# Kernel optimization log

Hardware: AMD Instinct MI355X
Metric: run time of the kernel (lower is better)

The kernel has to match this reference:

```python
import jax, jax.numpy as jnp
import numpy as np

N_EMBD = 1024
N_HEAD = 16
HEAD_SIZE = N_EMBD // N_HEAD
EPS = 1e-5


def _layernorm(x, g, b):
    m = x.mean(-1, keepdims=True)
    v = x.var(-1, keepdims=True)
    return (x - m) / jnp.sqrt(v + EPS) * g + b


def _mha(q_in, kv_in, wq, wk, wv, pw, pb, causal):
    # q_in: [B,T,C], kv_in: [B,S,C]; per-head Linear projections fused into one matmul.
    B, T, C = q_in.shape
    S = kv_in.shape[1]
    H, hd = N_HEAD, HEAD_SIZE
    q = (q_in @ wq).reshape(B, T, H, hd)
    k = (kv_in @ wk).reshape(B, S, H, hd)
    v = (kv_in @ wv).reshape(B, S, H, hd)
    scale = 1.0 / np.sqrt(hd).astype(np.float32)
    wei = jnp.einsum('bthd,bshd->bhts', q, k) * scale  # [B,H,T,S]
    if causal:
        mask = jnp.tril(jnp.ones((T, S), dtype=bool))
        wei = jnp.where(mask, wei, -jnp.inf)
    attn = jax.nn.softmax(wei, axis=-1)
    out = jnp.einsum('bhts,bshd->bthd', attn, v).reshape(B, T, C)
    return out @ pw + pb


def setup_inputs() -> dict:
    key = jax.random.key(0)
    ks = jax.random.split(key, 20)
    C = N_EMBD
    B, T, S = 8, 1024, 1024
    s = 0.02
    inp = {
        'x': jax.random.normal(ks[0], (B, T, C), jnp.float32),
        'encoder_output': jax.random.normal(ks[1], (B, S, C), jnp.float32),
        # self-attention (per-head q/k/v Linears concatenated head-major -> [C, C])
        'sa_wq': jax.random.normal(ks[2], (C, C), jnp.float32) * s,
        'sa_wk': jax.random.normal(ks[3], (C, C), jnp.float32) * s,
        'sa_wv': jax.random.normal(ks[4], (C, C), jnp.float32) * s,
        'sa_pw': jax.random.normal(ks[5], (C, C), jnp.float32) * s,
        'sa_pb': jnp.zeros((C,), jnp.float32),
        # cross-attention
        'ca_wq': jax.random.normal(ks[6], (C, C), jnp.float32) * s,
        'ca_wk': jax.random.normal(ks[7], (C, C), jnp.float32) * s,
        'ca_wv': jax.random.normal(ks[8], (C, C), jnp.float32) * s,
        'ca_pw': jax.random.normal(ks[9], (C, C), jnp.float32) * s,
        'ca_pb': jnp.zeros((C,), jnp.float32),
        # feed-forward
        'ff_w1': jax.random.normal(ks[10], (C, 4 * C), jnp.float32) * s,
        'ff_b1': jnp.zeros((4 * C,), jnp.float32),
        'ff_w2': jax.random.normal(ks[11], (4 * C, C), jnp.float32) * s,
        'ff_b2': jnp.zeros((C,), jnp.float32),
        # layernorms
        'ln1_g': jnp.ones((C,), jnp.float32), 'ln1_b': jnp.zeros((C,), jnp.float32),
        'ln2_g': jnp.ones((C,), jnp.float32), 'ln2_b': jnp.zeros((C,), jnp.float32),
        'ln3_g': jnp.ones((C,), jnp.float32), 'ln3_b': jnp.zeros((C,), jnp.float32),
    }
    return inp


def reference(x, encoder_output, sa_wq, sa_wk, sa_wv, sa_pw, sa_pb,
              ca_wq, ca_wk, ca_wv, ca_pw, ca_pb,
              ff_w1, ff_b1, ff_w2, ff_b2,
              ln1_g, ln1_b, ln2_g, ln2_b, ln3_g, ln3_b):
    # self-attn: q from ln1(x), but k/v from raw residual x (memory=x in source)
    x = x + _mha(_layernorm(x, ln1_g, ln1_b), x, sa_wq, sa_wk, sa_wv, sa_pw, sa_pb, causal=True)
    # cross-attn: q from ln2(x), k/v from encoder_output, no mask
    x = x + _mha(_layernorm(x, ln2_g, ln2_b), encoder_output, ca_wq, ca_wk, ca_wv, ca_pw, ca_pb, causal=False)
    # feed-forward: Linear -> ReLU -> Linear
    h = _layernorm(x, ln3_g, ln3_b)
    x = x + (jax.nn.relu(h @ ff_w1 + ff_b1) @ ff_w2 + ff_b2)
    return x
```

## Files before the change

### kernel.cpp

```cpp
#include <hip/hip_runtime.h>
#include <stdint.h>
#include <stddef.h>

typedef __bf16 bf16_t;
typedef __bf16 bf16x4 __attribute__((ext_vector_type(4)));
typedef __bf16 bf16x8 __attribute__((ext_vector_type(8)));
typedef float f32x4 __attribute__((ext_vector_type(4)));

#define DEV static __device__ __forceinline__

static constexpr int kB = 8, kT = 1024, kC = 1024, kM = 8192, kH = 16, kHD = 64, kFF = 4096;

DEV f32x4 mfma16(bf16x8 a, bf16x8 b, f32x4 c) {
  return __builtin_amdgcn_mfma_f32_16x16x32_bf16(a, b, c, 0, 0, 0);
}

DEV float ex2(float x) {
  float r;
  asm("v_exp_f32 %0, %1" : "=v"(r) : "v"(x));
  return r;
}

DEV void gload_lds16(const void* g, void* l) {
  __builtin_amdgcn_global_load_lds(
      reinterpret_cast<const __attribute__((address_space(1))) void*>(
          reinterpret_cast<uintptr_t>(g)),
      reinterpret_cast<__attribute__((address_space(3))) void*>(
          static_cast<uint32_t>(reinterpret_cast<uintptr_t>(l))),
      16, 0, 0);
}

__global__ void k_cast_bf16(const float* __restrict__ in, bf16_t* __restrict__ out, int n4) {
  int i = blockIdx.x * blockDim.x + threadIdx.x;
  if (i >= n4) return;
  float4 v = reinterpret_cast<const float4*>(in)[i];
  bf16x4 o;
  o[0] = (bf16_t)v.x; o[1] = (bf16_t)v.y; o[2] = (bf16_t)v.z; o[3] = (bf16_t)v.w;
  reinterpret_cast<bf16x4*>(out)[i] = o;
}

struct Trans8Args { const float* src[8]; bf16_t* dst[8]; };
__global__ void k_transpose_cast8(Trans8Args a) {
  __shared__ float tile[32][33];
  const float* __restrict__ in = a.src[blockIdx.z];
  bf16_t* __restrict__ out = a.dst[blockIdx.z];
  int c0 = blockIdx.x * 32, r0 = blockIdx.y * 32;
  int tx = threadIdx.x, ty = threadIdx.y;
#pragma unroll
  for (int i = 0; i < 4; ++i)
    tile[ty + 8 * i][tx] = in[(size_t)(r0 + ty + 8 * i) * kC + c0 + tx];
  __syncthreads();
#pragma unroll
  for (int i = 0; i < 4; ++i)
    out[(size_t)(c0 + ty + 8 * i) * kC + r0 + tx] = (bf16_t)tile[tx][ty + 8 * i];
}

__global__ void k_transpose_cast(const float* __restrict__ in, bf16_t* __restrict__ out,
                                 int R, int C) {
  __shared__ float tile[32][33];
  int c0 = blockIdx.x * 32, r0 = blockIdx.y * 32;
  int tx = threadIdx.x, ty = threadIdx.y;
#pragma unroll
  for (int i = 0; i < 4; ++i)
    tile[ty + 8 * i][tx] = in[(size_t)(r0 + ty + 8 * i) * C + c0 + tx];
  __syncthreads();
#pragma unroll
  for (int i = 0; i < 4; ++i)
    out[(size_t)(c0 + ty + 8 * i) * R + r0 + tx] = (bf16_t)tile[tx][ty + 8 * i];
}

template <bool CASTX>
__global__ __launch_bounds__(256) void k_ln(const float* __restrict__ in,
                                            const float* __restrict__ g,
                                            const float* __restrict__ b,
                                            bf16_t* __restrict__ out,
                                            bf16_t* __restrict__ rawout) {
  int row = blockIdx.x, t = threadIdx.x;
  const float4 v = reinterpret_cast<const float4*>(in + (size_t)row * kC)[t];
  if constexpr (CASTX) {
    bf16x4 c;
    c[0] = (bf16_t)v.x; c[1] = (bf16_t)v.y; c[2] = (bf16_t)v.z; c[3] = (bf16_t)v.w;
    reinterpret_cast<bf16x4*>(rawout + (size_t)row * kC)[t] = c;
  }
  float s = v.x + v.y + v.z + v.w;
  float ss = v.x * v.x + v.y * v.y + v.z * v.z + v.w * v.w;
#pragma unroll
  for (int off = 1; off < 64; off <<= 1) {
    s += __shfl_xor(s, off, 64);
    ss += __shfl_xor(ss, off, 64);
  }
  __shared__ float rs[4], rss[4];
  int w = t >> 6;
  if ((t & 63) == 0) { rs[w] = s; rss[w] = ss; }
  __syncthreads();
  s = rs[0] + rs[1] + rs[2] + rs[3];
  ss = rss[0] + rss[1] + rss[2] + rss[3];
  float mean = s * (1.f / kC);
  float var = ss * (1.f / kC) - mean * mean;
  float rstd = rsqrtf(var + 1e-5f);
  float4 gv = reinterpret_cast<const float4*>(g)[t];
  float4 bv = reinterpret_cast<const float4*>(b)[t];
  bf16x4 o;
  o[0] = (bf16_t)((v.x - mean) * rstd * gv.x + bv.x);
  o[1] = (bf16_t)((v.y - mean) * rstd * gv.y + bv.y);
  o[2] = (bf16_t)((v.z - mean) * rstd * gv.z + bv.z);
  o[3] = (bf16_t)((v.w - mean) * rstd * gv.w + bv.w);
  reinterpret_cast<bf16x4*>(out + (size_t)row * kC)[t] = o;
}

template <int EPI>
__global__ __launch_bounds__(512, 2) void k_gemm2(
    const bf16_t* __restrict__ A, const bf16_t* __restrict__ Bt,
    const float* __restrict__ bias, const float* __restrict__ res,
    float* __restrict__ outf, bf16_t* __restrict__ outb, bf16_t* __restrict__ outb2,
    int M, int N, int K) {
  extern __shared__ bf16_t smem[];
  bf16_t* As = smem;
  bf16_t* Bs = smem + 3 * 8192;
  const int t = threadIdx.x;
  const int w = t >> 6, lane = t & 63;
  const int l15 = lane & 15, l4 = lane >> 4;
  const int wr = w >> 2, wc = w & 3;
  const int bm0 = blockIdx.y * 128, bn0 = blockIdx.x * 256;

  f32x4 acc[4][4] = {};

  const int srow = w * 8 + (lane >> 3);
  const int scol = ((lane & 7) ^ (lane >> 3)) * 8;
  const bf16_t* aSrc0 = A + (size_t)(bm0 + srow) * K + scol;
  const bf16_t* bSrc0 = Bt + (size_t)(bn0 + srow) * K + scol;
  const size_t r64 = (size_t)64 * K;

  const int arow = wr * 64 + l15;
  const int brow = wc * 64 + l15;
  const int cbx = (l15 & 7) * 16;
  const int cbe0 = ((l4 * 16) ^ cbx) >> 1;
  const int cbe1 = ((64 | (l4 * 16)) ^ cbx) >> 1;

  const int nkt = K >> 6;

  auto stage = [&](int tt, int bi) {
    const size_t ko = (size_t)tt * 64;
    bf16_t* da = As + bi * 8192;
    bf16_t* db = Bs + bi * 16384;
    gload_lds16(aSrc0 + ko,            da + w * 512);
    gload_lds16(aSrc0 + ko + r64,      da + 4096 + w * 512);
    gload_lds16(bSrc0 + ko,            db + w * 512);
    gload_lds16(bSrc0 + ko + r64,      db + 4096 + w * 512);
    gload_lds16(bSrc0 + ko + 2 * r64,  db + 8192 + w * 512);
    gload_lds16(bSrc0 + ko + 3 * r64,  db + 12288 + w * 512);
  };

  stage(0, 0);
  stage(1, 1);
  asm volatile("s_waitcnt vmcnt(6)" ::: "memory");
  __builtin_amdgcn_s_barrier();

  int bi = 0, bs = 2;
  for (int tt = 0; tt < nkt; ++tt) {
    if (tt + 2 < nkt) stage(tt + 2, bs);
    const bf16_t* bA = As + bi * 8192;
    const bf16_t* bB = Bs + bi * 16384;
    bf16x8 af[4], bfr[4];
#pragma unroll
    for (int m = 0; m < 4; ++m)
      af[m] = *reinterpret_cast<const bf16x8*>(&bA[(arow + m * 16) * 64 + cbe0]);
#pragma unroll
    for (int n = 0; n < 4; ++n)
      bfr[n] = *reinterpret_cast<const bf16x8*>(&bB[(brow + n * 16) * 64 + cbe0]);
    __builtin_amdgcn_s_setprio(1);
#pragma unroll
    for (int m = 0; m < 4; ++m)
#pragma unroll
      for (int n = 0; n < 4; ++n) acc[m][n] = mfma16(af[m], bfr[n], acc[m][n]);
    __builtin_amdgcn_s_setprio(0);
#pragma unroll
    for (int m = 0; m < 4; ++m)
      af[m] = *reinterpret_cast<const bf16x8*>(&bA[(arow + m * 16) * 64 + cbe1]);
#pragma unroll
    for (int n = 0; n < 4; ++n)
      bfr[n] = *reinterpret_cast<const bf16x8*>(&bB[(brow + n * 16) * 64 + cbe1]);
    __builtin_amdgcn_s_setprio(1);
#pragma unroll
    for (int m = 0; m < 4; ++m)
#pragma unroll
      for (int n = 0; n < 4; ++n) acc[m][n] = mfma16(af[m], bfr[n], acc[m][n]);
    __builtin_amdgcn_s_setprio(0);
    if (tt + 1 < nkt) {
      if (tt + 2 < nkt) asm volatile("s_waitcnt vmcnt(6)" ::: "memory");
      else              asm volatile("s_waitcnt vmcnt(0)" ::: "memory");
      __builtin_amdgcn_s_barrier();
    }
    bi = (bi == 2) ? 0 : bi + 1;
    bs = (bs == 2) ? 0 : bs + 1;
  }

  const int gm = bm0 + wr * 64 + l4 * 4;
  const int gn = bn0 + wc * 64 + l15;
  if constexpr (EPI == 0) {
#pragma unroll
    for (int m = 0; m < 4; ++m)
#pragma unroll
      for (int n = 0; n < 4; ++n)
#pragma unroll
        for (int r = 0; r < 4; ++r)
          outb[(size_t)(gm + m * 16 + r) * N + (gn + n * 16)] = (bf16_t)acc[m][n][r];
  } else if constexpr (EPI == 1) {
#pragma unroll
    for (int m = 0; m < 4; ++m)
#pragma unroll
      for (int n = 0; n < 4; ++n) {
        const int col = gn + n * 16;
        const float bv = bias[col];
#pragma unroll
        for (int r = 0; r < 4; ++r) {
          const size_t idx = (size_t)(gm + m * 16 + r) * N + col;
          outf[idx] = acc[m][n][r] + bv + res[idx];
        }
      }
  } else if constexpr (EPI == 2) {
#pragma unroll
    for (int m = 0; m < 4; ++m)
#pragma unroll
      for (int n = 0; n < 4; ++n) {
        const int col = gn + n * 16;
        const float bv = bias[col];
#pragma unroll
        for (int r = 0; r < 4; ++r) {
          float v = acc[m][n][r] + bv;
          v = fmaxf(v, 0.f);
          outb[(size_t)(gm + m * 16 + r) * N + col] = (bf16_t)v;
        }
      }
  } else if constexpr (EPI == 3) {
#pragma unroll
    for (int m = 0; m < 4; ++m)
#pragma unroll
      for (int n = 0; n < 4; ++n) {
        bf16x4 ov;
#pragma unroll
        for (int r = 0; r < 4; ++r) ov[r] = (bf16_t)acc[m][n][r];
        *reinterpret_cast<bf16x4*>(&outb[(size_t)(gn + n * 16) * M + gm + m * 16]) = ov;
      }
  } else {
    const int half = N >> 1;
    if (bn0 < half) {
#pragma unroll
      for (int m = 0; m < 4; ++m)
#pragma unroll
        for (int n = 0; n < 4; ++n)
#pragma unroll
          for (int r = 0; r < 4; ++r)
            outb[(size_t)(gm + m * 16 + r) * half + (gn + n * 16)] = (bf16_t)acc[m][n][r];
    } else {
#pragma unroll
      for (int m = 0; m < 4; ++m)
#pragma unroll
        for (int n = 0; n < 4; ++n) {
          bf16x4 ov;
#pragma unroll
          for (int r = 0; r < 4; ++r) ov[r] = (bf16_t)acc[m][n][r];
          *reinterpret_cast<bf16x4*>(
              &outb2[(size_t)(gn + n * 16 - half) * M + gm + m * 16]) = ov;
        }
    }
  }
}

template <bool CAUSAL>
__global__ __launch_bounds__(256) void k_attn(const bf16_t* __restrict__ Q,
                                              const bf16_t* __restrict__ Kb,
                                              const bf16_t* __restrict__ Vt,
                                              bf16_t* __restrict__ O) {
  __shared__ bf16_t Ks[2][4096];
  __shared__ bf16_t Vs[2][4096];
  __shared__ bf16_t P[4][32][72];
  const int b = blockIdx.x, h = blockIdx.y;
  const int w = threadIdx.x >> 6, lane = threadIdx.x & 63;
  const int l15 = lane & 15, l4 = lane >> 4;
  const int qblk = CAUSAL ? (kT / 128 - 1 - blockIdx.z) : blockIdx.z;
  const int qr0 = qblk * 128 + w * 32;

  bf16x8 qf[2][2];
#pragma unroll
  for (int a = 0; a < 2; ++a) {
    const bf16_t* qp = Q + (size_t)(b * kT + qr0 + a * 16 + l15) * kC + h * kHD + l4 * 8;
    qf[a][0] = *reinterpret_cast<const bf16x8*>(qp);
    qf[a][1] = *reinterpret_cast<const bf16x8*>(qp + 32);
#pragma unroll
    for (int j = 0; j < 8; ++j) {
      qf[a][0][j] = (bf16_t)((float)qf[a][0][j] * 0.1803368801111204f);
      qf[a][1][j] = (bf16_t)((float)qf[a][1][j] * 0.1803368801111204f);
    }
  }
  bf16x8 ones;
#pragma unroll
  for (int j = 0; j < 8; ++j) ones[j] = (bf16_t)1.0f;

  f32x4 po[2][4] = {};
  f32x4 po_s[2] = {};
  float mrun[2];
  mrun[0] = mrun[1] = -3.0e38f;

  const int nkt = CAUSAL ? 2 * qblk + 2 : (kT / 64);
  const int klim = CAUSAL ? ((qr0 + 31) >> 6) : (1 << 30);

  const int lr = lane >> 3;
  const int cswz = ((lane & 7) ^ lr) * 8;
  const bf16_t* kSrc0 = Kb + (size_t)(b * kT + 2 * w * 8 + lr) * kC + h * kHD + cswz;
  const bf16_t* kSrc1 = Kb + (size_t)(b * kT + (2 * w + 1) * 8 + lr) * kC + h * kHD + cswz;
  const bf16_t* vSrc0 = Vt + (size_t)(h * kHD + 2 * w * 8 + lr) * (kB * kT) + b * kT + cswz;
  const bf16_t* vSrc1 = Vt + (size_t)(h * kHD + (2 * w + 1) * 8 + lr) * (kB * kT) + b * kT + cswz;

  auto stage = [&](int kt, int buf) {
    const size_t kk = (size_t)kt * 64 * kC;
    const size_t vv = (size_t)kt * 64;
    gload_lds16(kSrc0 + kk, &Ks[buf][(2 * w) * 512]);
    gload_lds16(kSrc1 + kk, &Ks[buf][(2 * w + 1) * 512]);
    gload_lds16(vSrc0 + vv, &Vs[buf][(2 * w) * 512]);
    gload_lds16(vSrc1 + vv, &Vs[buf][(2 * w + 1) * 512]);
  };

  const int cbx = (l15 & 7) * 16;
  const int rb0 = ((l4 * 16) ^ cbx) >> 1;
  const int rb1 = ((64 | (l4 * 16)) ^ cbx) >> 1;

  stage(0, 0);
  asm volatile("s_waitcnt vmcnt(0)" ::: "memory");
  __builtin_amdgcn_s_barrier();

  int buf = 0;
  for (int kt = 0; kt < nkt; ++kt) {
    if (kt + 1 < nkt) stage(kt + 1, buf ^ 1);
    if (kt <= klim) {
      bf16x8 kf[4][2];
#pragma unroll
      for (int sub = 0; sub < 4; ++sub) {
        kf[sub][0] = *reinterpret_cast<const bf16x8*>(&Ks[buf][(sub * 16 + l15) * 64 + rb0]);
        kf[sub][1] = *reinterpret_cast<const bf16x8*>(&Ks[buf][(sub * 16 + l15) * 64 + rb1]);
      }
      bf16x8 vf[2][4];
#pragma unroll
      for (int n = 0; n < 4; ++n) {
        vf[0][n] = *reinterpret_cast<const bf16x8*>(&Vs[buf][(n * 16 + l15) * 64 + rb0]);
        vf[1][n] = *reinterpret_cast<const bf16x8*>(&Vs[buf][(n * 16 + l15) * 64 + rb1]);
      }

      f32x4 s[2][4] = {};
      __builtin_amdgcn_s_setprio(1);
#pragma unroll
      for (int a = 0; a < 2; ++a)
#pragma unroll
        for (int sub = 0; sub < 4; ++sub) {
          s[a][sub] = mfma16(kf[sub][0], qf[a][0], s[a][sub]);
          s[a][sub] = mfma16(kf[sub][1], qf[a][1], s[a][sub]);
        }
      __builtin_amdgcn_s_setprio(0);
      if (CAUSAL && kt == klim) {
#pragma unroll
        for (int a = 0; a < 2; ++a) {
          const int qrow = qr0 + a * 16 + l15;
#pragma unroll
          for (int sub = 0; sub < 4; ++sub)
#pragma unroll
            for (int r = 0; r < 4; ++r) {
              const int key = kt * 64 + sub * 16 + l4 * 4 + r;
              if (key > qrow) s[a][sub][r] = -3.0e38f;
            }
        }
      }
#pragma unroll
      for (int a = 0; a < 2; ++a) {
        float t0 = fmaxf(fmaxf(s[a][0][0], s[a][0][1]), fmaxf(s[a][0][2], s[a][0][3]));
        float t1 = fmaxf(fmaxf(s[a][1][0], s[a][1][1]), fmaxf(s[a][1][2], s[a][1][3]));
        float t2 = fmaxf(fmaxf(s[a][2][0], s[a][2][1]), fmaxf(s[a][2][2], s[a][2][3]));
        float t3 = fmaxf(fmaxf(s[a][3][0], s[a][3][1]), fmaxf(s[a][3][2], s[a][3][3]));
        float v = fmaxf(fmaxf(t0, t1), fmaxf(t2, t3));
        v = fmaxf(v, __shfl_xor(v, 16, 64));
        v = fmaxf(v, __shfl_xor(v, 32, 64));
        if (!__all(v <= mrun[a] + 8.f)) {
          const float mnew = fmaxf(mrun[a], v);
          const float corr = ex2(mrun[a] - mnew);
          mrun[a] = mnew;
#pragma unroll
          for (int n = 0; n < 4; ++n)
#pragma unroll
            for (int r = 0; r < 4; ++r) po[a][n][r] *= corr;
#pragma unroll
          for (int r = 0; r < 4; ++r) po_s[a][r] *= corr;
        }
#pragma unroll
        for (int sub = 0; sub < 4; ++sub) {
          bf16x4 pk;
#pragma unroll
          for (int r = 0; r < 4; ++r) pk[r] = (bf16_t)ex2(s[a][sub][r] - mrun[a]);
          *reinterpret_cast<bf16x4*>(&P[w][a * 16 + l15][sub * 16 + l4 * 4]) = pk;
        }
      }
#pragma unroll
      for (int a = 0; a < 2; ++a)
#pragma unroll
        for (int kk = 0; kk < 2; ++kk) {
          const bf16x8 pf =
              *reinterpret_cast<const bf16x8*>(&P[w][a * 16 + l15][kk * 32 + l4 * 8]);
          __builtin_amdgcn_s_setprio(1);
#pragma unroll
          for (int n = 0; n < 4; ++n) po[a][n] = mfma16(vf[kk][n], pf, po[a][n]);
          po_s[a] = mfma16(ones, pf, po_s[a]);
          __builtin_amdgcn_s_setprio(0);
        }
    }
    asm volatile("s_waitcnt vmcnt(0)" ::: "memory");
    __builtin_amdgcn_s_barrier();
    buf ^= 1;
  }

#pragma unroll
  for (int a = 0; a < 2; ++a) {
    const float inv = 1.f / po_s[a][0];
#pragma unroll
    for (int n = 0; n < 4; ++n) {
      bf16x4 ov;
#pragma unroll
      for (int r = 0; r < 4; ++r) ov[r] = (bf16_t)(po[a][n][r] * inv);
      *reinterpret_cast<bf16x4*>(
          O + (size_t)(b * kT + qr0 + a * 16 + l15) * kC + h * kHD + n * 16 + l4 * 4) = ov;
    }
  }
}

extern "C" void kernel_launch(void* const* d_in, const int* in_sizes, int n_in,
                              void* d_out, int out_size, void* d_ws, size_t ws_size,
                              hipStream_t stream) {
  const float* x      = (const float*)d_in[0];
  const float* enc    = (const float*)d_in[1];
  const float* sa_wq  = (const float*)d_in[2];
  const float* sa_wk  = (const float*)d_in[3];
  const float* sa_wv  = (const float*)d_in[4];
  const float* sa_pw  = (const float*)d_in[5];
  const float* sa_pb  = (const float*)d_in[6];
  const float* ca_wq  = (const float*)d_in[7];
  const float* ca_wk  = (const float*)d_in[8];
  const float* ca_wv  = (const float*)d_in[9];
  const float* ca_pw  = (const float*)d_in[10];
  const float* ca_pb  = (const float*)d_in[11];
  const float* ff_w1  = (const float*)d_in[12];
  const float* ff_b1  = (const float*)d_in[13];
  const float* ff_w2  = (const float*)d_in[14];
  const float* ff_b2  = (const float*)d_in[15];
  const float* ln1_g  = (const float*)d_in[16];
  const float* ln1_b  = (const float*)d_in[17];
  const float* ln2_g  = (const float*)d_in[18];
  const float* ln2_b  = (const float*)d_in[19];
  const float* ln3_g  = (const float*)d_in[20];
  const float* ln3_b  = (const float*)d_in[21];

  const size_t ACT_BF = (size_t)kM * kC * 2;
  const size_t ACT_F  = (size_t)kM * kC * 4;
  const size_t W_BF   = (size_t)kC * kC * 2;
  const size_t FF_BF  = (size_t)kC * kFF * 2;
  const size_t H_BF   = (size_t)kM * kFF * 2;

  char* ws = (char*)d_ws;
  size_t off = 0;
  auto alloc = [&](size_t bytes) {
    char* p = ws + off;
    off += (bytes + 255) & ~(size_t)255;
    return p;
  };
  bf16_t* xbf   = (bf16_t*)alloc(ACT_BF);
  bf16_t* encbf = (bf16_t*)alloc(ACT_BF);
  bf16_t* lnbuf = (bf16_t*)alloc(ACT_BF);
  bf16_t* wsaq  = (bf16_t*)alloc(W_BF);
  bf16_t* wkvsa = (bf16_t*)alloc(2 * W_BF);
  bf16_t* wsap  = (bf16_t*)alloc(W_BF);
  bf16_t* wcaq  = (bf16_t*)alloc(W_BF);
  bf16_t* wkvca = (bf16_t*)alloc(2 * W_BF);
  bf16_t* wcap  = (bf16_t*)alloc(W_BF);
  bf16_t* wff1t = (bf16_t*)alloc(FF_BF);
  bf16_t* wff2t = (bf16_t*)alloc(FF_BF);
  float*  rbuf  = (float*)alloc(ACT_F);
  char*   scr   = alloc(5 * ACT_BF > H_BF ? 5 * ACT_BF : H_BF);
  bf16_t* qbf   = (bf16_t*)scr;
  bf16_t* kbf   = (bf16_t*)(scr + ACT_BF);
  bf16_t* vtbf  = (bf16_t*)(scr + 3 * ACT_BF);
  bf16_t* aobf  = (bf16_t*)(scr + 4 * ACT_BF);
  bf16_t* hbf   = (bf16_t*)scr;

  const dim3 blk512(512), blk256(256), blkT(32, 8);
  const int n4 = kM * kC / 4;
  const dim3 gGemmC(kC / 256, kM / 128);
  const dim3 gGemmKV(2 * kC / 256, kM / 128);
  const dim3 gGemmF(kFF / 256, kM / 128);
  const dim3 gAttn(kB, kH, kT / 128);
  const uint32_t LDSB = 147456;

  hipFuncSetAttribute((const void*)k_gemm2<0>, hipFuncAttributeMaxDynamicSharedMemorySize, LDSB);
  hipFuncSetAttribute((const void*)k_gemm2<1>, hipFuncAttributeMaxDynamicSharedMemorySize, LDSB);
  hipFuncSetAttribute((const void*)k_gemm2<2>, hipFuncAttributeMaxDynamicSharedMemorySize, LDSB);
  hipFuncSetAttribute((const void*)k_gemm2<4>, hipFuncAttributeMaxDynamicSharedMemorySize, LDSB);

  k_cast_bf16<<<n4 / 256, blk256, 0, stream>>>(enc, encbf, n4);
  Trans8Args ta;
  ta.src[0] = sa_wq; ta.dst[0] = wsaq;
  ta.src[1] = sa_wk; ta.dst[1] = wkvsa;
  ta.src[2] = sa_wv; ta.dst[2] = wkvsa + (size_t)kC * kC;
  ta.src[3] = sa_pw; ta.dst[3] = wsap;
  ta.src[4] = ca_wq; ta.dst[4] = wcaq;
  ta.src[5] = ca_wk; ta.dst[5] = wkvca;
  ta.src[6] = ca_wv; ta.dst[6] = wkvca + (size_t)kC * kC;
  ta.src[7] = ca_pw; ta.dst[7] = wcap;
  k_transpose_cast8<<<dim3(kC / 32, kC / 32, 8), blkT, 0, stream>>>(ta);
  k_transpose_cast<<<dim3(kFF / 32, kC / 32), blkT, 0, stream>>>(ff_w1, wff1t, kC, kFF);
  k_transpose_cast<<<dim3(kC / 32, kFF / 32), blkT, 0, stream>>>(ff_w2, wff2t, kFF, kC);

  k_ln<true><<<kM, blk256, 0, stream>>>(x, ln1_g, ln1_b, lnbuf, xbf);
  k_gemm2<0><<<gGemmC, blk512, LDSB, stream>>>(lnbuf, wsaq, nullptr, nullptr, nullptr, qbf, nullptr, kM, kC, kC);
  k_gemm2<4><<<gGemmKV, blk512, LDSB, stream>>>(xbf, wkvsa, nullptr, nullptr, nullptr, kbf, vtbf, kM, 2 * kC, kC);
  k_attn<true><<<gAttn, blk256, 0, stream>>>(qbf, kbf, vtbf, aobf);
  k_gemm2<1><<<gGemmC, blk512, LDSB, stream>>>(aobf, wsap, sa_pb, x, rbuf, nullptr, nullptr, kM, kC, kC);

  k_ln<false><<<kM, blk256, 0, stream>>>(rbuf, ln2_g, ln2_b, lnbuf, nullptr);
  k_gemm2<0><<<gGemmC, blk512, LDSB, stream>>>(lnbuf, wcaq, nullptr, nullptr, nullptr, qbf, nullptr, kM, kC, kC);
  k_gemm2<4><<<gGemmKV, blk512, LDSB, stream>>>(encbf, wkvca, nullptr, nullptr, nullptr, kbf, vtbf, kM, 2 * kC, kC);
  k_attn<false><<<gAttn, blk256, 0, stream>>>(qbf, kbf, vtbf, aobf);
  k_gemm2<1><<<gGemmC, blk512, LDSB, stream>>>(aobf, wcap, ca_pb, rbuf, rbuf, nullptr, nullptr, kM, kC, kC);

  k_ln<false><<<kM, blk256, 0, stream>>>(rbuf, ln3_g, ln3_b, lnbuf, nullptr);
  k_gemm2<2><<<gGemmF, blk512, LDSB, stream>>>(lnbuf, wff1t, ff_b1, nullptr, nullptr, hbf, nullptr, kM, kFF, kC);
  k_gemm2<1><<<gGemmC, blk512, LDSB, stream>>>(hbf, wff2t, ff_b2, rbuf, (float*)d_out, nullptr, nullptr, kM, kC, kFF);

  (void)in_sizes; (void)n_in; (void)out_size; (void)ws_size;
}
```

Baseline: 515.0 us.

## Add 256x256-tile GEMM kernel with split-half pipelining for KV and FF1 projections

Introduces k_gemm3, a 256x256 output tile GEMM with 8 waves (each computing 128x64) that double-buffers A and B in LDS and stages the next K tile in four quarter loads interleaved with MFMA phases. It replaces the 128-row k_gemm2 for the wide KV projections and the FF1 layer, aiming to raise arithmetic intensity and cut global/LDS traffic per FLOP. The larger accumulator footprint (128 floats per thread) raises register pressure and halves the grid size, which could hurt occupancy or tail balance.

```diff
diff --git a/kernel.cpp b/kernel.cpp
--- a/kernel.cpp
+++ b/kernel.cpp
@@ -255,6 +255,172 @@
     } else {
 #pragma unroll
       for (int m = 0; m < 4; ++m)
+#pragma unroll
+        for (int n = 0; n < 4; ++n) {
+          bf16x4 ov;
+#pragma unroll
+          for (int r = 0; r < 4; ++r) ov[r] = (bf16_t)acc[m][n][r];
+          *reinterpret_cast<bf16x4*>(
+              &outb2[(size_t)(gn + n * 16 - half) * M + gm + m * 16]) = ov;
+        }
+    }
+  }
+}
+
+template <int EPI>
+__global__ __launch_bounds__(512, 2) void k_gemm3(
+    const bf16_t* __restrict__ A, const bf16_t* __restrict__ Bt,
+    const float* __restrict__ bias,
+    bf16_t* __restrict__ outb, bf16_t* __restrict__ outb2,
+    int M, int N, int K) {
+  extern __shared__ bf16_t smem[];
+  bf16_t* As = smem;
+  bf16_t* Bs = smem + 32768;
+  const int t = threadIdx.x;
+  const int w = t >> 6, lane = t & 63;
+  const int l15 = lane & 15, l4 = lane >> 4;
+  const int wr = w >> 2, wc = w & 3;
+  const int bm0 = blockIdx.y * 256, bn0 = blockIdx.x * 256;
+
+  f32x4 acc[8][4] = {};
+
+  const int srow = w * 8 + (lane >> 3);
+  const int scol = ((lane & 7) ^ (lane >> 3)) * 8;
+  const bf16_t* aSrc0 = A + (size_t)(bm0 + srow) * K + scol;
+  const bf16_t* bSrc0 = Bt + (size_t)(bn0 + srow) * K + scol;
+  const size_t r64 = (size_t)64 * K;
+
+  const int arow = wr * 128 + l15;
+  const int brow = wc * 64 + l15;
+  const int cbx = (l15 & 7) * 16;
+  const int cbe0 = ((l4 * 16) ^ cbx) >> 1;
+  const int cbe1 = ((64 | (l4 * 16)) ^ cbx) >> 1;
+
+  const int nkt = K >> 6;
+
+  auto stage_half = [&](int tt, int h, int bi) {
+    const size_t ko = (size_t)tt * 64;
+    if (h < 2) {
+      bf16_t* d = As + bi * 16384 + h * 8192 + w * 512;
+      gload_lds16(aSrc0 + ko + (size_t)(2 * h) * r64,     d);
+      gload_lds16(aSrc0 + ko + (size_t)(2 * h + 1) * r64, d + 4096);
+    } else {
+      const int hh = h - 2;
+      bf16_t* d = Bs + bi * 16384 + hh * 8192 + w * 512;
+      gload_lds16(bSrc0 + ko + (size_t)(2 * hh) * r64,     d);
+      gload_lds16(bSrc0 + ko + (size_t)(2 * hh + 1) * r64, d + 4096);
+    }
+  };
+
+  stage_half(0, 0, 0); stage_half(0, 1, 0); stage_half(0, 2, 0); stage_half(0, 3, 0);
+  if (nkt > 1) {
+    stage_half(1, 0, 1); stage_half(1, 1, 1);
+    asm volatile("s_waitcnt vmcnt(4)" ::: "memory");
+  } else {
+    asm volatile("s_waitcnt vmcnt(0)" ::: "memory");
+  }
+  __builtin_amdgcn_s_barrier();
+
+  for (int tt = 0; tt < nkt; ++tt) {
+    const int bi = tt & 1;
+    const bf16_t* bA = As + bi * 16384;
+    const bf16_t* bB = Bs + bi * 16384;
+    bf16x8 aK0lo[4], aK0hi[4], aK1lo[4], aK1hi[4], bK0[4], bK1[4];
+
+#pragma unroll
+    for (int m = 0; m < 4; ++m)
+      aK0lo[m] = *reinterpret_cast<const bf16x8*>(&bA[(arow + m * 16) * 64 + cbe0]);
+#pragma unroll
+    for (int n = 0; n < 4; ++n)
+      bK0[n] = *reinterpret_cast<const bf16x8*>(&bB[(brow + n * 16) * 64 + cbe0]);
+    if (tt + 1 < nkt) stage_half(tt + 1, 2, bi ^ 1);
+    __builtin_amdgcn_s_barrier();
+    asm volatile("s_waitcnt lgkmcnt(0)" ::: "memory");
+    __builtin_amdgcn_s_setprio(1);
+#pragma unroll
+    for (int m = 0; m < 4; ++m)
+#pragma unroll
+      for (int n = 0; n < 4; ++n) acc[m][n] = mfma16(aK0lo[m], bK0[n], acc[m][n]);
+    __builtin_amdgcn_s_setprio(0);
+    __builtin_amdgcn_s_barrier();
+
+#pragma unroll
+    for (int m = 0; m < 4; ++m)
+      aK0hi[m] = *reinterpret_cast<const bf16x8*>(&bA[(arow + 64 + m * 16) * 64 + cbe0]);
+    if (tt + 1 < nkt) stage_half(tt + 1, 3, bi ^ 1);
+    __builtin_amdgcn_s_barrier();
+    asm volatile("s_waitcnt lgkmcnt(0)" ::: "memory");
+    __builtin_amdgcn_s_setprio(1);
+#pragma unroll
+    for (int m = 0; m < 4; ++m)
+#pragma unroll
+      for (int n = 0; n < 4; ++n) acc[4 + m][n] = mfma16(aK0hi[m], bK0[n], acc[4 + m][n]);
+    __builtin_amdgcn_s_setprio(0);
+    __builtin_amdgcn_s_barrier();
+
+#pragma unroll
+    for (int m = 0; m < 4; ++m)
+      aK1lo[m] = *reinterpret_cast<const bf16x8*>(&bA[(arow + m * 16) * 64 + cbe1]);
+#pragma unroll
+    for (int m = 0; m < 4; ++m)
+      aK1hi[m] = *reinterpret_cast<const bf16x8*>(&bA[(arow + 64 + m * 16) * 64 + cbe1]);
+#pragma unroll
+    for (int n = 0; n < 4; ++n)
+      bK1[n] = *reinterpret_cast<const bf16x8*>(&bB[(brow + n * 16) * 64 + cbe1]);
+    __builtin_amdgcn_s_barrier();
+    asm volatile("s_waitcnt lgkmcnt(0)" ::: "memory");
+    __builtin_amdgcn_s_setprio(1);
+#pragma unroll
+    for (int m = 0; m < 4; ++m)
+#pragma unroll
+      for (int n = 0; n < 4; ++n) acc[m][n] = mfma16(aK1lo[m], bK1[n], acc[m][n]);
+    __builtin_amdgcn_s_setprio(0);
+    __builtin_amdgcn_s_barrier();
+
+    if (tt + 2 < nkt) { stage_half(tt + 2, 0, bi); stage_half(tt + 2, 1, bi); }
+    if (tt + 1 < nkt) {
+      if (tt + 2 < nkt) asm volatile("s_waitcnt vmcnt(4)" ::: "memory");
+      else              asm volatile("s_waitcnt vmcnt(0)" ::: "memory");
+    }
+    __builtin_amdgcn_s_barrier();
+    __builtin_amdgcn_s_setprio(1);
+#pragma unroll
+    for (int m = 0; m < 4; ++m)
+#pragma unroll
+      for (int n = 0; n < 4; ++n) acc[4 + m][n] = mfma16(aK1hi[m], bK1[n], acc[4 + m][n]);
+    __builtin_amdgcn_s_setprio(0);
+    __builtin_amdgcn_s_barrier();
+  }
+
+  const int gm = bm0 + wr * 128 + l4 * 4;
+  const int gn = bn0 + wc * 64 + l15;
+  if constexpr (EPI == 2) {
+#pragma unroll
+    for (int m = 0; m < 8; ++m)
+#pragma unroll
+      for (int n = 0; n < 4; ++n) {
+        const int col = gn + n * 16;
+        const float bv = bias[col];
+#pragma unroll
+        for (int r = 0; r < 4; ++r) {
+          float v = acc[m][n][r] + bv;
+          v = fmaxf(v, 0.f);
+          outb[(size_t)(gm + m * 16 + r) * N + col] = (bf16_t)v;
+        }
+      }
+  } else {
+    const int half = N >> 1;
+    if (bn0 < half) {
+#pragma unroll
+      for (int m = 0; m < 8; ++m)
+#pragma unroll
+        for (int n = 0; n < 4; ++n)
+#pragma unroll
+          for (int r = 0; r < 4; ++r)
+            outb[(size_t)(gm + m * 16 + r) * half + (gn + n * 16)] = (bf16_t)acc[m][n][r];
+    } else {
+#pragma unroll
+      for (int m = 0; m < 8; ++m)
 #pragma unroll
         for (int n = 0; n < 4; ++n) {
           bf16x4 ov;
@@ -490,15 +656,17 @@
   const dim3 blk512(512), blk256(256), blkT(32, 8);
   const int n4 = kM * kC / 4;
   const dim3 gGemmC(kC / 256, kM / 128);
-  const dim3 gGemmKV(2 * kC / 256, kM / 128);
-  const dim3 gGemmF(kFF / 256, kM / 128);
+  const dim3 gGemmF2(kC / 256, kM / 128);
+  const dim3 gKV3(2 * kC / 256, kM / 256);
+  const dim3 gFF13(kFF / 256, kM / 256);
   const dim3 gAttn(kB, kH, kT / 128);
-  const uint32_t LDSB = 147456;
-
-  hipFuncSetAttribute((const void*)k_gemm2<0>, hipFuncAttributeMaxDynamicSharedMemorySize, LDSB);
-  hipFuncSetAttribute((const void*)k_gemm2<1>, hipFuncAttributeMaxDynamicSharedMemorySize, LDSB);
-  hipFuncSetAttribute((const void*)k_gemm2<2>, hipFuncAttributeMaxDynamicSharedMemorySize, LDSB);
-  hipFuncSetAttribute((const void*)k_gemm2<4>, hipFuncAttributeMaxDynamicSharedMemorySize, LDSB);
+  const uint32_t LDSB2 = 147456;
+  const uint32_t LDSB3 = 131072;
+
+  hipFuncSetAttribute((const void*)k_gemm2<0>, hipFuncAttributeMaxDynamicSharedMemorySize, LDSB2);
+  hipFuncSetAttribute((const void*)k_gemm2<1>, hipFuncAttributeMaxDynamicSharedMemorySize, LDSB2);
+  hipFuncSetAttribute((const void*)k_gemm3<2>, hipFuncAttributeMaxDynamicSharedMemorySize, LDSB3);
+  hipFuncSetAttribute((const void*)k_gemm3<4>, hipFuncAttributeMaxDynamicSharedMemorySize, LDSB3);
 
   k_cast_bf16<<<n4 / 256, blk256, 0, stream>>>(enc, encbf, n4);
   Trans8Args ta;
@@ -515,20 +683,20 @@
   k_transpose_cast<<<dim3(kC / 32, kFF / 32), blkT, 0, stream>>>(ff_w2, wff2t, kFF, kC);
 
   k_ln<true><<<kM, blk256, 0, stream>>>(x, ln1_g, ln1_b, lnbuf, xbf);
-  k_gemm2<0><<<gGemmC, blk512, LDSB, stream>>>(lnbuf, wsaq, nullptr, nullptr, nullptr, qbf, nullptr, kM, kC, kC);
-  k_gemm2<4><<<gGemmKV, blk512, LDSB, stream>>>(xbf, wkvsa, nullptr, nullptr, nullptr, kbf, vtbf, kM, 2 * kC, kC);
+  k_gemm2<0><<<gGemmC, blk512, LDSB2, stream>>>(lnbuf, wsaq, nullptr, nullptr, nullptr, qbf, nullptr, kM, kC, kC);
+  k_gemm3<4><<<gKV3, blk512, LDSB3, stream>>>(xbf, wkvsa, nullptr, kbf, vtbf, kM, 2 * kC, kC);
   k_attn<true><<<gAttn, blk256, 0, stream>>>(qbf, kbf, vtbf, aobf);
-  k_gemm2<1><<<gGemmC, blk512, LDSB, stream>>>(aobf, wsap, sa_pb, x, rbuf, nullptr, nullptr, kM, kC, kC);
+  k_gemm2<1><<<gGemmC, blk512, LDSB2, stream>>>(aobf, wsap, sa_pb, x, rbuf, nullptr, nullptr, kM, kC, kC);
 
   k_ln<false><<<kM, blk256, 0, stream>>>(rbuf, ln2_g, ln2_b, lnbuf, nullptr);
-  k_gemm2<0><<<gGemmC, blk512, LDSB, stream>>>(lnbuf, wcaq, nullptr, nullptr, nullptr, qbf, nullptr, kM, kC, kC);
-  k_gemm2<4><<<gGemmKV, blk512, LDSB, stream>>>(encbf, wkvca, nullptr, nullptr, nullptr, kbf, vtbf, kM, 2 * kC, kC);
+  k_gemm2<0><<<gGemmC, blk512, LDSB2, stream>>>(lnbuf, wcaq, nullptr, nullptr, nullptr, qbf, nullptr, kM, kC, kC);
+  k_gemm3<4><<<gKV3, blk512, LDSB3, stream>>>(encbf, wkvca, nullptr, kbf, vtbf, kM, 2 * kC, kC);
   k_attn<false><<<gAttn, blk256, 0, stream>>>(qbf, kbf, vtbf, aobf);
-  k_gemm2<1><<<gGemmC, blk512, LDSB, stream>>>(aobf, wcap, ca_pb, rbuf, rbuf, nullptr, nullptr, kM, kC, kC);
+  k_gemm2<1><<<gGemmC, blk512, LDSB2, stream>>>(aobf, wcap, ca_pb, rbuf, rbuf, nullptr, nullptr, kM, kC, kC);
 
   k_ln<false><<<kM, blk256, 0, stream>>>(rbuf, ln3_g, ln3_b, lnbuf, nullptr);
-  k_gemm2<2><<<gGemmF, blk512, LDSB, stream>>>(lnbuf, wff1t, ff_b1, nullptr, nullptr, hbf, nullptr, kM, kFF, kC);
-  k_gemm2<1><<<gGemmC, blk512, LDSB, stream>>>(hbf, wff2t, ff_b2, rbuf, (float*)d_out, nullptr, nullptr, kM, kC, kFF);
+  k_gemm3<2><<<gFF13, blk512, LDSB3, stream>>>(lnbuf, wff1t, ff_b1, hbf, nullptr, kM, kFF, kC);
+  k_gemm2<1><<<gGemmF2, blk512, LDSB2, stream>>>(hbf, wff2t, ff_b2, rbuf, (float*)d_out, nullptr, nullptr, kM, kC, kFF);
 
   (void)in_sizes; (void)n_in; (void)out_size; (void)ws_size;
 }
```

Result: faster. 504.5 us (-2.1%).

## Shrink GEMM tile to 128x128 with 4 waves and double buffering

Applied to the files above, without the earlier changes.

The GEMM kernel moves from a 128x256 tile with 8 waves and triple-buffered LDS to a 128x128 tile with 4 waves and double buffering. LDS use drops from 147456 to 65536 bytes, so more blocks can be resident per CU and the grid doubles in size. The cost is less operand reuse per loaded byte and a shallower prefetch pipeline that waits with vmcnt(0) every iteration, which may expose global-load latency.

```diff
diff --git a/kernel.cpp b/kernel.cpp
--- a/kernel.cpp
+++ b/kernel.cpp
@@ -109,19 +109,19 @@
 }
 
 template <int EPI>
-__global__ __launch_bounds__(512, 2) void k_gemm2(
+__global__ __launch_bounds__(256, 2) void k_gemm2(
     const bf16_t* __restrict__ A, const bf16_t* __restrict__ Bt,
     const float* __restrict__ bias, const float* __restrict__ res,
     float* __restrict__ outf, bf16_t* __restrict__ outb, bf16_t* __restrict__ outb2,
     int M, int N, int K) {
   extern __shared__ bf16_t smem[];
   bf16_t* As = smem;
-  bf16_t* Bs = smem + 3 * 8192;
+  bf16_t* Bs = smem + 2 * 8192;
   const int t = threadIdx.x;
   const int w = t >> 6, lane = t & 63;
   const int l15 = lane & 15, l4 = lane >> 4;
-  const int wr = w >> 2, wc = w & 3;
-  const int bm0 = blockIdx.y * 128, bn0 = blockIdx.x * 256;
+  const int wr = w >> 1, wc = w & 1;
+  const int bm0 = blockIdx.y * 128, bn0 = blockIdx.x * 128;
 
   f32x4 acc[4][4] = {};
 
@@ -129,7 +129,7 @@
   const int scol = ((lane & 7) ^ (lane >> 3)) * 8;
   const bf16_t* aSrc0 = A + (size_t)(bm0 + srow) * K + scol;
   const bf16_t* bSrc0 = Bt + (size_t)(bn0 + srow) * K + scol;
-  const size_t r64 = (size_t)64 * K;
+  const size_t r32 = (size_t)32 * K;
 
   const int arow = wr * 64 + l15;
   const int brow = wc * 64 + l15;
@@ -141,26 +141,24 @@
 
   auto stage = [&](int tt, int bi) {
     const size_t ko = (size_t)tt * 64;
-    bf16_t* da = As + bi * 8192;
-    bf16_t* db = Bs + bi * 16384;
-    gload_lds16(aSrc0 + ko,            da + w * 512);
-    gload_lds16(aSrc0 + ko + r64,      da + 4096 + w * 512);
-    gload_lds16(bSrc0 + ko,            db + w * 512);
-    gload_lds16(bSrc0 + ko + r64,      db + 4096 + w * 512);
-    gload_lds16(bSrc0 + ko + 2 * r64,  db + 8192 + w * 512);
-    gload_lds16(bSrc0 + ko + 3 * r64,  db + 12288 + w * 512);
+    bf16_t* da = As + bi * 8192 + w * 512;
+    bf16_t* db = Bs + bi * 8192 + w * 512;
+#pragma unroll
+    for (int c = 0; c < 4; ++c) {
+      gload_lds16(aSrc0 + ko + (size_t)c * r32, da + c * 2048);
+      gload_lds16(bSrc0 + ko + (size_t)c * r32, db + c * 2048);
+    }
   };
 
   stage(0, 0);
-  stage(1, 1);
-  asm volatile("s_waitcnt vmcnt(6)" ::: "memory");
+  asm volatile("s_waitcnt vmcnt(0)" ::: "memory");
   __builtin_amdgcn_s_barrier();
 
-  int bi = 0, bs = 2;
+  int bi = 0;
   for (int tt = 0; tt < nkt; ++tt) {
-    if (tt + 2 < nkt) stage(tt + 2, bs);
+    if (tt + 1 < nkt) stage(tt + 1, bi ^ 1);
     const bf16_t* bA = As + bi * 8192;
-    const bf16_t* bB = Bs + bi * 16384;
+    const bf16_t* bB = Bs + bi * 8192;
     bf16x8 af[4], bfr[4];
 #pragma unroll
     for (int m = 0; m < 4; ++m)
@@ -187,12 +185,10 @@
       for (int n = 0; n < 4; ++n) acc[m][n] = mfma16(af[m], bfr[n], acc[m][n]);
     __builtin_amdgcn_s_setprio(0);
     if (tt + 1 < nkt) {
-      if (tt + 2 < nkt) asm volatile("s_waitcnt vmcnt(6)" ::: "memory");
-      else              asm volatile("s_waitcnt vmcnt(0)" ::: "memory");
+      asm volatile("s_waitcnt vmcnt(0)" ::: "memory");
       __builtin_amdgcn_s_barrier();
     }
-    bi = (bi == 2) ? 0 : bi + 1;
-    bs = (bs == 2) ? 0 : bs + 1;
+    bi ^= 1;
   }
 
   const int gm = bm0 + wr * 64 + l4 * 4;
@@ -487,13 +483,13 @@
   bf16_t* aobf  = (bf16_t*)(scr + 4 * ACT_BF);
   bf16_t* hbf   = (bf16_t*)scr;
 
-  const dim3 blk512(512), blk256(256), blkT(32, 8);
+  const dim3 blk256(256), blkT(32, 8);
   const int n4 = kM * kC / 4;
-  const dim3 gGemmC(kC / 256, kM / 128);
-  const dim3 gGemmKV(2 * kC / 256, kM / 128);
-  const dim3 gGemmF(kFF / 256, kM / 128);
+  const dim3 gGemmC(kC / 128, kM / 128);
+  const dim3 gGemmKV(2 * kC / 128, kM / 128);
+  const dim3 gGemmF(kFF / 128, kM / 128);
   const dim3 gAttn(kB, kH, kT / 128);
-  const uint32_t LDSB = 147456;
+  const uint32_t LDSB = 65536;
 
   hipFuncSetAttribute((const void*)k_gemm2<0>, hipFuncAttributeMaxDynamicSharedMemorySize, LDSB);
   hipFuncSetAttribute((const void*)k_gemm2<1>, hipFuncAttributeMaxDynamicSharedMemorySize, LDSB);
@@ -515,20 +511,20 @@
   k_transpose_cast<<<dim3(kC / 32, kFF / 32), blkT, 0, stream>>>(ff_w2, wff2t, kFF, kC);
 
   k_ln<true><<<kM, blk256, 0, stream>>>(x, ln1_g, ln1_b, lnbuf, xbf);
-  k_gemm2<0><<<gGemmC, blk512, LDSB, stream>>>(lnbuf, wsaq, nullptr, nullptr, nullptr, qbf, nullptr, kM, kC, kC);
-  k_gemm2<4><<<gGemmKV, blk512, LDSB, stream>>>(xbf, wkvsa, nullptr, nullptr, nullptr, kbf, vtbf, kM, 2 * kC, kC);
+  k_gemm2<0><<<gGemmC, blk256, LDSB, stream>>>(lnbuf, wsaq, nullptr, nullptr, nullptr, qbf, nullptr, kM, kC, kC);
+  k_gemm2<4><<<gGemmKV, blk256, LDSB, stream>>>(xbf, wkvsa, nullptr, nullptr, nullptr, kbf, vtbf, kM, 2 * kC, kC);
   k_attn<true><<<gAttn, blk256, 0, stream>>>(qbf, kbf, vtbf, aobf);
-  k_gemm2<1><<<gGemmC, blk512, LDSB, stream>>>(aobf, wsap, sa_pb, x, rbuf, nullptr, nullptr, kM, kC, kC);
+  k_gemm2<1><<<gGemmC, blk256, LDSB, stream>>>(aobf, wsap, sa_pb, x, rbuf, nullptr, nullptr, kM, kC, kC);
 
   k_ln<false><<<kM, blk256, 0, stream>>>(rbuf, ln2_g, ln2_b, lnbuf, nullptr);
-  k_gemm2<0><<<gGemmC, blk512, LDSB, stream>>>(lnbuf, wcaq, nullptr, nullptr, nullptr, qbf, nullptr, kM, kC, kC);
-  k_gemm2<4><<<gGemmKV, blk512, LDSB, stream>>>(encbf, wkvca, nullptr, nullptr, nullptr, kbf, vtbf, kM, 2 * kC, kC);
+  k_gemm2<0><<<gGemmC, blk256, LDSB, stream>>>(lnbuf, wcaq, nullptr, nullptr, nullptr, qbf, nullptr, kM, kC, kC);
+  k_gemm2<4><<<gGemmKV, blk256, LDSB, stream>>>(encbf, wkvca, nullptr, nullptr, nullptr, kbf, vtbf, kM, 2 * kC, kC);
   k_attn<false><<<gAttn, blk256, 0, stream>>>(qbf, kbf, vtbf, aobf);
-  k_gemm2<1><<<gGemmC, blk512, LDSB, stream>>>(aobf, wcap, ca_pb, rbuf, rbuf, nullptr, nullptr, kM, kC, kC);
+  k_gemm2<1><<<gGemmC, blk256, LDSB, stream>>>(aobf, wcap, ca_pb, rbuf, rbuf, nullptr, nullptr, kM, kC, kC);
 
   k_ln<false><<<kM, blk256, 0, stream>>>(rbuf, ln3_g, ln3_b, lnbuf, nullptr);
-  k_gemm2<2><<<gGemmF, blk512, LDSB, stream>>>(lnbuf, wff1t, ff_b1, nullptr, nullptr, hbf, nullptr, kM, kFF, kC);
-  k_gemm2<1><<<gGemmC, blk512, LDSB, stream>>>(hbf, wff2t, ff_b2, rbuf, (float*)d_out, nullptr, nullptr, kM, kC, kFF);
+  k_gemm2<2><<<gGemmF, blk256, LDSB, stream>>>(lnbuf, wff1t, ff_b1, nullptr, nullptr, hbf, nullptr, kM, kFF, kC);
+  k_gemm2<1><<<gGemmC, blk256, LDSB, stream>>>(hbf, wff2t, ff_b2, rbuf, (float*)d_out, nullptr, nullptr, kM, kC, kFF);
 
   (void)in_sizes; (void)n_in; (void)out_size; (void)ws_size;
 }
```

After: 514.5 us. No clear change (-0.1%).
